# Optimization experiments

Hardware: AMD Instinct MI355X
Metric: run time of the kernel (lower is better)

The kernel has to match this reference:

```python
import jax, jax.numpy as jnp
import numpy as np

VEC_SIZE = 128
N_VECS = 8
N_ROWS = 256  # n_choices * redundancy
BATCH = 512
EPS = 1e-8


def _combos(n):
    # combos[i, j] = 0 if bit j of i is set else 1  -> shape [2^n, n]
    i = np.arange(2 ** n)[:, None]
    j = np.arange(n)[None, :]
    return jnp.asarray(((i >> j) & 1) == 0, dtype=jnp.float32)


def setup_inputs() -> dict:
    key = jax.random.key(0)
    kq, kw = jax.random.split(key)
    query = jax.random.normal(kq, (BATCH, N_VECS * VEC_SIZE), dtype=jnp.float32)
    weight = jax.random.normal(kw, (N_ROWS, N_VECS * VEC_SIZE), dtype=jnp.float32)
    # match torch init: weight rows normalized over full flattened dim
    weight = weight / jnp.clip(jnp.linalg.norm(weight, axis=1, keepdims=True), EPS)
    return {"query": query, "weight": weight}


def reference(query, weight):
    combos = _combos(N_VECS)                               # [C, n]  C = 2^n
    q = query.reshape(-1, N_VECS, VEC_SIZE)                # [b, n, v]
    w = weight.reshape(-1, N_VECS, VEC_SIZE)               # [r, n, v]
    # cosine similarity over vec_size, per (batch row, weight row, vec slot)
    dot = jnp.einsum('bnv,rnv->brn', q, w)                 # [b, r, n]
    qn = jnp.maximum(jnp.linalg.norm(q, axis=-1), EPS)     # [b, n]
    wn = jnp.maximum(jnp.linalg.norm(w, axis=-1), EPS)     # [r, n]
    cos_sim = dot / (qn[:, None, :] * wn[None, :, :])
    cos_sim = jax.nn.relu(cos_sim)                         # [b, r, n]
    # NAND combo interpolation then product over the n_vecs axis
    cs = cos_sim[:, :, None, :]                            # [b, r, 1, n]
    c = combos[None, None, :, :]                           # [1, 1, C, n]
    transformed = c * cs + (1.0 - c) * (1.0 - cs)          # [b, r, C, n]
    return jnp.prod(transformed, axis=-1)                  # [b, r, C]
```

## Files before the change

kernel.cpp:

```cpp
#include <hip/hip_runtime.h>
#include <math.h>

#define BATCH  512
#define NROWS  256
#define NVECS  8
#define VSIZE  128
#define DIM    1024
#define NCOMBO 256

typedef float vf4 __attribute__((ext_vector_type(4)));

__global__ __launch_bounds__(256) void prescale_kernel(
    const float* __restrict__ q, const float* __restrict__ w,
    float* __restrict__ qn, float* __restrict__ wn) {
  int wid  = (blockIdx.x * 256 + threadIdx.x) >> 6;
  int lane = threadIdx.x & 63;
  const float* src; float* dst;
  if (wid < BATCH * NVECS) {
    src = q  + (size_t)wid * VSIZE;
    dst = qn + (size_t)wid * VSIZE;
  } else {
    int k = wid - BATCH * NVECS;
    src = w  + (size_t)k * VSIZE;
    dst = wn + (size_t)k * VSIZE;
  }
  float2 v = *(const float2*)(src + lane * 2);
  float ss = fmaf(v.x, v.x, v.y * v.y);
  #pragma unroll
  for (int m = 1; m <= 32; m <<= 1) ss += __shfl_xor(ss, m, 64);
  float inv = 1.0f / fmaxf(sqrtf(ss), 1e-8f);
  float2 o; o.x = v.x * inv; o.y = v.y * inv;
  *(float2*)(dst + lane * 2) = o;
}

__global__ __launch_bounds__(256) void fused_kernel(
    const float* __restrict__ q, const float* __restrict__ w,
    float* __restrict__ out) {
  __shared__ __align__(16) float Ws[8 * 1056];
  __shared__ __align__(16) float CS[64][8];
  const int t  = threadIdx.x;
  const int wv = t >> 6, lane = t & 63;
  const int bs = blockIdx.x * 8, rs = blockIdx.y * 8;

  #pragma unroll
  for (int i = 0; i < 8; ++i) {
    int f = i * 256 + t;
    int g = f << 2;
    int row = g >> 10, e = g & 1023;
    float4 v = *(const float4*)(w + (size_t)(rs + row) * DIM + e);
    *(float4*)(Ws + row * 1056 + (e >> 7) * 132 + (e & 127)) = v;
  }

  const int n = lane >> 3, c = lane & 7;
  const int koff = n * VSIZE + c * 16;

  float4 qa[4], qb[4];
  {
    const float* Q0 = q + (size_t)(bs + 2 * wv) * DIM + koff;
    #pragma unroll
    for (int j = 0; j < 4; ++j) {
      qa[j] = *(const float4*)(Q0 + 4 * j);
      qb[j] = *(const float4*)(Q0 + DIM + 4 * j);
    }
  }
  __syncthreads();

  const float* Wb = Ws + n * 132 + c * 16;
  #pragma unroll
  for (int r = 0; r < 8; ++r) {
    const float* Wr = Wb + r * 1056;
    float s0 = 0.f, s1 = 0.f;
    #pragma unroll
    for (int j = 0; j < 4; ++j) {
      float4 w4 = *(const float4*)(Wr + 4 * j);
      s0 = fmaf(qa[j].x, w4.x, s0); s0 = fmaf(qa[j].y, w4.y, s0);
      s0 = fmaf(qa[j].z, w4.z, s0); s0 = fmaf(qa[j].w, w4.w, s0);
      s1 = fmaf(qb[j].x, w4.x, s1); s1 = fmaf(qb[j].y, w4.y, s1);
      s1 = fmaf(qb[j].z, w4.z, s1); s1 = fmaf(qb[j].w, w4.w, s1);
    }
    #pragma unroll
    for (int m = 1; m <= 4; m <<= 1) {
      s0 += __shfl_xor(s0, m, 64);
      s1 += __shfl_xor(s1, m, 64);
    }
    if (c < 2) {
      float v = (c == 0) ? s0 : s1;
      CS[(2 * wv + c) * 8 + r][n] = fmaxf(v, 0.f);
    }
  }
  __syncthreads();

  #pragma unroll 4
  for (int i = 0; i < 16; ++i) {
    int p = wv * 16 + i;
    int bl = p >> 3, r = p & 7;
    float4 cA = *(const float4*)(&CS[p][0]);
    float4 cB = *(const float4*)(&CS[p][4]);
    float t2 = (lane & 1)  ? 1.f - cA.z : cA.z;
    float t3 = (lane & 2)  ? 1.f - cA.w : cA.w;
    float t4 = (lane & 4)  ? 1.f - cB.x : cB.x;
    float t5 = (lane & 8)  ? 1.f - cB.y : cB.y;
    float t6 = (lane & 16) ? 1.f - cB.z : cB.z;
    float t7 = (lane & 32) ? 1.f - cB.w : cB.w;
    float base = ((t2 * t3) * (t4 * t5)) * (t6 * t7);
    float c0 = cA.x, c1 = cA.y;
    vf4 o;
    o.x = base * (c0 * c1);
    o.y = base * ((1.f - c0) * c1);
    o.z = base * (c0 * (1.f - c1));
    o.w = base * ((1.f - c0) * (1.f - c1));
    size_t off = ((size_t)(bs + bl) * NROWS + (rs + r)) * NCOMBO + lane * 4;
    __builtin_nontemporal_store(o, (vf4*)(out + off));
  }
}

extern "C" void kernel_launch(void* const* d_in, const int* in_sizes, int n_in,
                              void* d_out, int out_size, void* d_ws, size_t ws_size,
                              hipStream_t stream) {
  const float* query  = (const float*)d_in[0];
  const float* weight = (const float*)d_in[1];
  float* out = (float*)d_out;

  float* qn = (float*)d_ws;
  float* wn = qn + (size_t)BATCH * DIM;

  hipLaunchKernelGGL(prescale_kernel, dim3(1536), dim3(256), 0, stream,
                     query, weight, qn, wn);
  hipLaunchKernelGGL(fused_kernel, dim3(64, 32), dim3(256), 0, stream,
                     qn, wn, out);
}
```

Baseline: 148.2 us.

## Fuse vector normalization into main kernel and drop prescale pass

Removes the separate prescale kernel and instead computes per-slot query and weight norms inside the fused kernel from data already in registers and shared memory, scaling the dot products afterwards. This saves one kernel launch and a full read/write round trip of the normalized query and weight arrays through the workspace. In exchange, each block recomputes the weight norms redundantly and does some extra shuffles. The output store also changes from a nontemporal store to a plain vector store.

```diff
diff --git a/kernel.cpp b/kernel.cpp
--- a/kernel.cpp
+++ b/kernel.cpp
@@ -9,29 +9,6 @@
 #define NCOMBO 256
 
 typedef float vf4 __attribute__((ext_vector_type(4)));
-
-__global__ __launch_bounds__(256) void prescale_kernel(
-    const float* __restrict__ q, const float* __restrict__ w,
-    float* __restrict__ qn, float* __restrict__ wn) {
-  int wid  = (blockIdx.x * 256 + threadIdx.x) >> 6;
-  int lane = threadIdx.x & 63;
-  const float* src; float* dst;
-  if (wid < BATCH * NVECS) {
-    src = q  + (size_t)wid * VSIZE;
-    dst = qn + (size_t)wid * VSIZE;
-  } else {
-    int k = wid - BATCH * NVECS;
-    src = w  + (size_t)k * VSIZE;
-    dst = wn + (size_t)k * VSIZE;
-  }
-  float2 v = *(const float2*)(src + lane * 2);
-  float ss = fmaf(v.x, v.x, v.y * v.y);
-  #pragma unroll
-  for (int m = 1; m <= 32; m <<= 1) ss += __shfl_xor(ss, m, 64);
-  float inv = 1.0f / fmaxf(sqrtf(ss), 1e-8f);
-  float2 o; o.x = v.x * inv; o.y = v.y * inv;
-  *(float2*)(dst + lane * 2) = o;
-}
 
 __global__ __launch_bounds__(256) void fused_kernel(
     const float* __restrict__ q, const float* __restrict__ w,
@@ -55,21 +32,33 @@
   const int koff = n * VSIZE + c * 16;
 
   float4 qa[4], qb[4];
+  float qs0 = 0.f, qs1 = 0.f;
   {
     const float* Q0 = q + (size_t)(bs + 2 * wv) * DIM + koff;
     #pragma unroll
     for (int j = 0; j < 4; ++j) {
       qa[j] = *(const float4*)(Q0 + 4 * j);
       qb[j] = *(const float4*)(Q0 + DIM + 4 * j);
+      qs0 = fmaf(qa[j].x, qa[j].x, qs0); qs0 = fmaf(qa[j].y, qa[j].y, qs0);
+      qs0 = fmaf(qa[j].z, qa[j].z, qs0); qs0 = fmaf(qa[j].w, qa[j].w, qs0);
+      qs1 = fmaf(qb[j].x, qb[j].x, qs1); qs1 = fmaf(qb[j].y, qb[j].y, qs1);
+      qs1 = fmaf(qb[j].z, qb[j].z, qs1); qs1 = fmaf(qb[j].w, qb[j].w, qs1);
     }
   }
+  #pragma unroll
+  for (int m = 1; m <= 4; m <<= 1) {
+    qs0 += __shfl_xor(qs0, m, 64);
+    qs1 += __shfl_xor(qs1, m, 64);
+  }
+  const float iq0 = 1.0f / fmaxf(sqrtf(qs0), 1e-8f);
+  const float iq1 = 1.0f / fmaxf(sqrtf(qs1), 1e-8f);
   __syncthreads();
 
   const float* Wb = Ws + n * 132 + c * 16;
   #pragma unroll
   for (int r = 0; r < 8; ++r) {
     const float* Wr = Wb + r * 1056;
-    float s0 = 0.f, s1 = 0.f;
+    float s0 = 0.f, s1 = 0.f, wss = 0.f;
     #pragma unroll
     for (int j = 0; j < 4; ++j) {
       float4 w4 = *(const float4*)(Wr + 4 * j);
@@ -77,14 +66,18 @@
       s0 = fmaf(qa[j].z, w4.z, s0); s0 = fmaf(qa[j].w, w4.w, s0);
       s1 = fmaf(qb[j].x, w4.x, s1); s1 = fmaf(qb[j].y, w4.y, s1);
       s1 = fmaf(qb[j].z, w4.z, s1); s1 = fmaf(qb[j].w, w4.w, s1);
+      wss = fmaf(w4.x, w4.x, wss); wss = fmaf(w4.y, w4.y, wss);
+      wss = fmaf(w4.z, w4.z, wss); wss = fmaf(w4.w, w4.w, wss);
     }
     #pragma unroll
     for (int m = 1; m <= 4; m <<= 1) {
-      s0 += __shfl_xor(s0, m, 64);
-      s1 += __shfl_xor(s1, m, 64);
+      s0  += __shfl_xor(s0, m, 64);
+      s1  += __shfl_xor(s1, m, 64);
+      wss += __shfl_xor(wss, m, 64);
     }
+    const float iw = 1.0f / fmaxf(sqrtf(wss), 1e-8f);
     if (c < 2) {
-      float v = (c == 0) ? s0 : s1;
+      float v = (c == 0) ? s0 * iq0 * iw : s1 * iq1 * iw;
       CS[(2 * wv + c) * 8 + r][n] = fmaxf(v, 0.f);
     }
   }
@@ -104,13 +97,13 @@
     float t7 = (lane & 32) ? 1.f - cB.w : cB.w;
     float base = ((t2 * t3) * (t4 * t5)) * (t6 * t7);
     float c0 = cA.x, c1 = cA.y;
-    vf4 o;
+    float4 o;
     o.x = base * (c0 * c1);
     o.y = base * ((1.f - c0) * c1);
     o.z = base * (c0 * (1.f - c1));
     o.w = base * ((1.f - c0) * (1.f - c1));
     size_t off = ((size_t)(bs + bl) * NROWS + (rs + r)) * NCOMBO + lane * 4;
-    __builtin_nontemporal_store(o, (vf4*)(out + off));
+    *(float4*)(out + off) = o;
   }
 }
 
@@ -120,12 +113,8 @@
   const float* query  = (const float*)d_in[0];
   const float* weight = (const float*)d_in[1];
   float* out = (float*)d_out;
+  (void)d_ws; (void)ws_size;
 
-  float* qn = (float*)d_ws;
-  float* wn = qn + (size_t)BATCH * DIM;
-
-  hipLaunchKernelGGL(prescale_kernel, dim3(1536), dim3(256), 0, stream,
-                     query, weight, qn, wn);
   hipLaunchKernelGGL(fused_kernel, dim3(64, 32), dim3(256), 0, stream,
-                     qn, wn, out);
+                     query, weight, out);
 }
```

New measurement: 145.5 us. No clear change (-1.9%).
